# Kernel tuning notes

Measured on AMD Instinct MI355X. Metric: run time of the kernel, lower is better.

The kernel has to match this reference:

```python
import jax, jax.numpy as jnp
import numpy as np

N, E = 100000, 1600000
DIMS = [128, 64, 64, 64, 32]  # in, hid, hid, hid, out
NEG_SLOPE = 0.2               # GATv2Conv default negative_slope
ELU_ALPHA_OUT = float(DIMS[-1])  # nn.ELU(out_channels): alpha = out_channels


def setup_inputs() -> dict:
    key = jax.random.key(0)
    ks = jax.random.split(key, 16)
    inp = {
        "x": jax.random.normal(ks[0], (N, DIMS[0]), dtype=jnp.float32),
        "edge_index": jax.random.randint(ks[1], (2, E), 0, N, dtype=jnp.int64),
    }
    ki = 2
    for i in range(4):
        fin, fout = DIMS[i], DIMS[i + 1]
        s = 1.0 / np.sqrt(fin)
        inp[f"Wl{i+1}"] = jax.random.uniform(ks[ki], (fin, fout), jnp.float32, -s, s); ki += 1
        inp[f"Wr{i+1}"] = jax.random.uniform(ks[ki], (fin, fout), jnp.float32, -s, s); ki += 1
        inp[f"att{i+1}"] = jax.random.uniform(ks[ki], (fout,), jnp.float32, -s, s); ki += 1
    return inp


def gatv2_layer(x, src, dst, Wl, Wr, att):
    # single head, concat=False, no self-loops, no bias (per module config)
    xl = x @ Wl                                   # [N, F] source-side projection
    xr = x @ Wr                                   # [N, F] target-side projection
    e = jax.nn.leaky_relu(xl[src] + xr[dst], NEG_SLOPE)   # [E, F]
    score = e @ att                               # [E]
    # softmax over incoming edges of each destination node
    m = jax.ops.segment_max(score, dst, num_segments=N)    # [N]
    ex = jnp.exp(score - m[dst])                  # [E]
    denom = jax.ops.segment_sum(ex, dst, num_segments=N)   # [N]
    alpha = ex / (denom[dst] + 1e-16)             # [E]
    # scatter-add weighted source messages
    return jax.ops.segment_sum(xl[src] * alpha[:, None], dst, num_segments=N)


def reference(x, edge_index, Wl1, Wr1, att1, Wl2, Wr2, att2, Wl3, Wr3, att3, Wl4, Wr4, att4):
    src, dst = edge_index[0], edge_index[1]
    h = jax.nn.elu(gatv2_layer(x, src, dst, Wl1, Wr1, att1))
    h = jax.nn.elu(gatv2_layer(h, src, dst, Wl2, Wr2, att2))
    h = jax.nn.elu(gatv2_layer(h, src, dst, Wl3, Wr3, att3))
    h = gatv2_layer(h, src, dst, Wl4, Wr4, att4)
    # nn.ELU(out_channels) -> ELU with alpha = out_channels (faithful quirk)
    return jnp.where(h > 0, h, ELU_ALPHA_OUT * jnp.expm1(h))
```

## Files before the change

kernel.cpp:

```cpp
#include <hip/hip_runtime.h>
#include <math.h>

typedef __attribute__((ext_vector_type(8))) short bf16x8;
typedef __attribute__((ext_vector_type(4))) float f32x4;
typedef __attribute__((ext_vector_type(4))) _Float16 h4;

#define BSHIFT 7
#define CH 8192

__device__ inline unsigned short f32_to_bf16_bits(float f) {
    unsigned int u = __float_as_uint(f);
    unsigned int r = (u + 0x7fffu + ((u >> 16) & 1u)) >> 16;
    return (unsigned short)r;
}
__device__ inline float bf16_bits_to_f32(unsigned short h) {
    return __uint_as_float(((unsigned int)h) << 16);
}

#define SWZ_ADD(t, imm) \
    t += __int_as_float(__builtin_amdgcn_ds_swizzle(__float_as_int(t), imm))


__global__ __launch_bounds__(256) void bucket_hist(
    const int* __restrict__ dst, int* __restrict__ bcnt8, int E, int nb, int nbp)
{
    __shared__ int h[1024];
    for (int i = threadIdx.x; i < nb; i += 256) h[i] = 0;
    __syncthreads();
    int e0 = blockIdx.x * CH, e1 = min(e0 + CH, E);
    for (int e = e0 + (int)threadIdx.x; e < e1; e += 256)
        atomicAdd(&h[dst[e] >> BSHIFT], 1);
    __syncthreads();
    int* mycnt = bcnt8 + (blockIdx.x & 7) * nbp;
    for (int b = threadIdx.x; b < nb; b += 256) {
        int c = h[b];
        if (c) atomicAdd(&mycnt[b], c);
    }
}

__global__ void bucket_scan(const int* __restrict__ bcnt8, int* __restrict__ bbase,
                            int* __restrict__ bcur8, int* __restrict__ rowstart,
                            int nb, int nbp, int E, int N)
{
    __shared__ int sh[1024];
    int t = threadIdx.x;
    int g8[8];
    int tot = 0;
#pragma unroll
    for (int g = 0; g < 8; ++g) {
        int c = (t < nb) ? bcnt8[g * nbp + t] : 0;
        g8[g] = c; tot += c;
    }
    sh[t] = tot;
    __syncthreads();
    for (int d = 1; d < 1024; d <<= 1) {
        int a = (t >= d) ? sh[t - d] : 0;
        __syncthreads();
        sh[t] += a;
        __syncthreads();
    }
    int base = sh[t] - tot;
    if (t <= nb) bbase[t] = base;
    if (t < nb) {
        int run = base;
#pragma unroll
        for (int g = 0; g < 8; ++g) { bcur8[g * nbp + t] = run; run += g8[g]; }
    }
    if (t == 0) rowstart[N] = E;
}

__global__ __launch_bounds__(256) void bucket_scatter(
    const int* __restrict__ src, const int* __restrict__ dst,
    int* __restrict__ bcur8, unsigned* __restrict__ pairs, int E, int nb, int nbp)
{
    __shared__ int h[1024];
    for (int i = threadIdx.x; i < nb; i += 256) h[i] = 0;
    __syncthreads();
    int e0 = blockIdx.x * CH, e1 = min(e0 + CH, E);
    for (int e = e0 + (int)threadIdx.x; e < e1; e += 256)
        atomicAdd(&h[dst[e] >> BSHIFT], 1);
    __syncthreads();
    int* mycur = bcur8 + (blockIdx.x & 7) * nbp;
    for (int b = threadIdx.x; b < nb; b += 256) {
        int c = h[b];
        if (c) h[b] = atomicAdd(&mycur[b], c);
    }
    __syncthreads();
    for (int e = e0 + (int)threadIdx.x; e < e1; e += 256) {
        int d = dst[e];
        int pos = atomicAdd(&h[d >> BSHIFT], 1);
        pairs[pos] = ((unsigned)src[e] << BSHIFT) | (unsigned)(d & 127);
    }
}

__global__ __launch_bounds__(256) void bucket_finalize(
    const unsigned* __restrict__ pairs, const int* __restrict__ bbase,
    int* __restrict__ rowstart, int* __restrict__ csr_src, int N)
{
    __shared__ int h[128];
    __shared__ int sh[256];
    int b = blockIdx.x;
    int p0 = bbase[b], p1 = bbase[b + 1];
    int t = threadIdx.x;
    if (t < 128) h[t] = 0;
    __syncthreads();
    for (int e = p0 + t; e < p1; e += 256)
        atomicAdd(&h[pairs[e] & 127], 1);
    __syncthreads();
    int v = (t < 128) ? h[t] : 0;
    sh[t] = v;
    __syncthreads();
    for (int d = 1; d < 256; d <<= 1) {
        int a = (t >= d) ? sh[t - d] : 0;
        __syncthreads();
        sh[t] += a;
        __syncthreads();
    }
    if (t < 128) {
        int off = sh[t] - v;
        int node = (b << BSHIFT) + t;
        if (node < N) rowstart[node] = p0 + off;
        h[t] = p0 + off;
    }
    __syncthreads();
    for (int e = p0 + t; e < p1; e += 256) {
        unsigned pr = pairs[e];
        int pos = atomicAdd(&h[pr & 127], 1);
        csr_src[pos] = (int)(pr >> BSHIFT);
    }
}


__global__ void prepack_kernel(const float* __restrict__ Wl, const float* __restrict__ Wr,
                               unsigned short* __restrict__ pWl, unsigned short* __restrict__ pWr,
                               int FIN, int FOUT) {
    int NT = FOUT >> 4, NK = FIN >> 5;
    int part = NT * NK * 512;
    int i = blockIdx.x * blockDim.x + threadIdx.x;
    int m = i / part;
    if (m >= 2) return;
    int ii = i - m * part;
    int j = ii & 7;
    int lane = (ii >> 3) & 63;
    int rest = ii >> 9;
    int ks = rest % NK;
    int t = rest / NK;
    int k = ks * 32 + (lane >> 4) * 8 + j;
    int c = t * 16 + (lane & 15);
    const float* W = m ? Wr : Wl;
    unsigned short* P = m ? pWr : pWl;
    float w = W[(size_t)k * FOUT + c];
    unsigned short hi = f32_to_bf16_bits(w);
    unsigned short lo = f32_to_bf16_bits(w - bf16_bits_to_f32(hi));
    P[ii] = hi;
    P[part + ii] = lo;
}


template<int FIN, int FOUT>
__global__ __launch_bounds__(256) void proj_mfma_kernel(
    const float* __restrict__ x,
    const unsigned short* __restrict__ pWl, const unsigned short* __restrict__ pWr,
    const float* __restrict__ att,
    _Float16* __restrict__ xlh, float* __restrict__ xr,
    float* __restrict__ dl, float* __restrict__ dr, int n)
{
    constexpr int NT = FOUT >> 4;
    constexpr int NK = FIN >> 5;
    constexpr int PART = NT * NK * 512;
    const int wave = threadIdx.x >> 6;
    const int lane = threadIdx.x & 63;
    const int row0 = blockIdx.x * 64 + wave * 16;
    int arow = row0 + (lane & 15);
    if (arow >= n) arow = n - 1;
    const int khalf = lane >> 4;

    f32x4 accl[NT], accr[NT];
#pragma unroll
    for (int t = 0; t < NT; ++t) {
        accl[t] = (f32x4){0.f, 0.f, 0.f, 0.f};
        accr[t] = (f32x4){0.f, 0.f, 0.f, 0.f};
    }

    const float* xrow = x + (size_t)arow * FIN + khalf * 8;
#pragma unroll
    for (int ks = 0; ks < NK; ++ks) {
        float4 a0 = *(const float4*)(xrow + ks * 32);
        float4 a1 = *(const float4*)(xrow + ks * 32 + 4);
        float av[8] = {a0.x, a0.y, a0.z, a0.w, a1.x, a1.y, a1.z, a1.w};
        bf16x8 ah, al;
#pragma unroll
        for (int j = 0; j < 8; ++j) {
            unsigned short h = f32_to_bf16_bits(av[j]);
            ah[j] = (short)h;
            al[j] = (short)f32_to_bf16_bits(av[j] - bf16_bits_to_f32(h));
        }
#pragma unroll
        for (int t = 0; t < NT; ++t) {
            const unsigned short* bpl = pWl + ((size_t)(t * NK + ks) * 64 + lane) * 8;
            bf16x8 bh  = *(const bf16x8*)bpl;
            bf16x8 blo = *(const bf16x8*)(bpl + PART);
            accl[t] = __builtin_amdgcn_mfma_f32_16x16x32_bf16(ah, bh,  accl[t], 0, 0, 0);
            accl[t] = __builtin_amdgcn_mfma_f32_16x16x32_bf16(ah, blo, accl[t], 0, 0, 0);
            accl[t] = __builtin_amdgcn_mfma_f32_16x16x32_bf16(al, bh,  accl[t], 0, 0, 0);
            const unsigned short* bpr = pWr + ((size_t)(t * NK + ks) * 64 + lane) * 8;
            bh  = *(const bf16x8*)bpr;
            blo = *(const bf16x8*)(bpr + PART);
            accr[t] = __builtin_amdgcn_mfma_f32_16x16x32_bf16(ah, bh,  accr[t], 0, 0, 0);
            accr[t] = __builtin_amdgcn_mfma_f32_16x16x32_bf16(ah, blo, accr[t], 0, 0, 0);
            accr[t] = __builtin_amdgcn_mfma_f32_16x16x32_bf16(al, bh,  accr[t], 0, 0, 0);
        }
    }

    const int orow0 = row0 + khalf * 4;
    const int colb = lane & 15;
    float attc[NT];
#pragma unroll
    for (int t = 0; t < NT; ++t) attc[t] = att[t * 16 + colb];

#pragma unroll
    for (int t = 0; t < NT; ++t) {
        int col = t * 16 + colb;
#pragma unroll
        for (int r = 0; r < 4; ++r) {
            int rr = orow0 + r;
            if (rr < n) {
                xlh[(size_t)rr * FOUT + col] = (_Float16)accl[t][r];
                xr[(size_t)rr * FOUT + col] = accr[t][r];
            }
        }
    }
#pragma unroll
    for (int r = 0; r < 4; ++r) {
        float pl = 0.f, pr = 0.f;
#pragma unroll
        for (int t = 0; t < NT; ++t) { pl += accl[t][r] * attc[t]; pr += accr[t][r] * attc[t]; }
#pragma unroll
        for (int off = 1; off < 16; off <<= 1) {
            pl += __shfl_xor(pl, off);
            pr += __shfl_xor(pr, off);
        }
        int rr = orow0 + r;
        if (colb == 0 && rr < n) { dl[rr] = pl; dr[rr] = pr; }
    }
}


template<int F, int AMODE>
__global__ __launch_bounds__(256) void agg_kernel(
    const _Float16* __restrict__ xlh, const float* __restrict__ xr, const float* __restrict__ att,
    const float* __restrict__ dl, const float* __restrict__ dr,
    const int* __restrict__ rowstart, const int* __restrict__ csr_src,
    float* __restrict__ out, int n, int E)
{
    constexpr int LPE = F / 4;
    constexpr int LSH = (F == 64) ? 6 : 5;
    constexpr int NPG = 64 / LPE;

    int wv  = (blockIdx.x * blockDim.x + threadIdx.x) >> 6;
    int lane = threadIdx.x & 63;
    int grp = lane / LPE;
    int fl  = lane % LPE;
    int node = wv * NPG + grp;
    bool act = node < n;
    int nc = act ? node : 0;

    float4 xrv  = *(const float4*)&xr[((unsigned)nc << LSH) + fl * 4];
    float4 attv = *(const float4*)&att[fl * 4];
    float cdr = 0.6f * dr[nc];

    int s0 = rowstart[nc];
    int s1 = act ? rowstart[nc + 1] : s0;
    int s1c = min(max(s1 - 1, s0), E - 1);

    float m = -1e30f, mth = -1e30f, ssum = 0.f;
    float o0 = 0.f, o1 = 0.f, o2 = 0.f, o3 = 0.f;

    int ia = s0, ib = s0 + 1;
    int sva = csr_src[min(ia, s1c)];
    int svb = csr_src[min(ib, s1c)];
    float dla = dl[sva], dlb = dl[svb];
    h4 xa = *(const h4*)(xlh + (((unsigned)sva << LSH) + fl * 4));
    h4 xb = *(const h4*)(xlh + (((unsigned)svb << LSH) + fl * 4));

    while (ia < s1) {
        int nia = ia + 2, nib = ib + 2;
        int nsva = csr_src[min(nia, s1c)];
        int nsvb = csr_src[min(nib, s1c)];
        float ndla = dl[nsva], ndlb = dl[nsvb];
        h4 nxa = *(const h4*)(xlh + (((unsigned)nsva << LSH) + fl * 4));
        h4 nxb = *(const h4*)(xlh + (((unsigned)nsvb << LSH) + fl * 4));

        float xa0 = (float)xa[0], xa1 = (float)xa[1], xa2 = (float)xa[2], xa3 = (float)xa[3];
        float xb0 = (float)xb[0], xb1 = (float)xb[1], xb2 = (float)xb[2], xb3 = (float)xb[3];

        bool vb = ib < s1;
        float ta = attv.x * fabsf(xa0 + xrv.x)
                 + attv.y * fabsf(xa1 + xrv.y)
                 + attv.z * fabsf(xa2 + xrv.z)
                 + attv.w * fabsf(xa3 + xrv.w);
        float tb = attv.x * fabsf(xb0 + xrv.x)
                 + attv.y * fabsf(xb1 + xrv.y)
                 + attv.z * fabsf(xb2 + xrv.z)
                 + attv.w * fabsf(xb3 + xrv.w);
        SWZ_ADD(ta, 0x041F); SWZ_ADD(tb, 0x041F);
        SWZ_ADD(ta, 0x081F); SWZ_ADD(tb, 0x081F);
        SWZ_ADD(ta, 0x101F); SWZ_ADD(tb, 0x101F);
        if (LPE == 16) { SWZ_ADD(ta, 0x201F); SWZ_ADD(tb, 0x201F); }

        float pa = 0.6f * dla + cdr + 0.4f * ta;
        float pb = vb ? (0.6f * dlb + cdr + 0.4f * tb) : -1e30f;

        float pm = fmaxf(pa, pb);
        if (pm > mth) {
            float c = __expf(m - pm);
            ssum *= c; o0 *= c; o1 *= c; o2 *= c; o3 *= c;
            m = pm; mth = pm + 8.0f;
        }
        float wa = __expf(pa - m);
        float wb = __expf(pb - m);
        ssum += wa + wb;
        o0 += wa * xa0 + wb * xb0;
        o1 += wa * xa1 + wb * xb1;
        o2 += wa * xa2 + wb * xb2;
        o3 += wa * xa3 + wb * xb3;

        ia = nia; ib = nib;
        dla = ndla; dlb = ndlb; xa = nxa; xb = nxb;
    }

    float inv = 1.f / (ssum + 1e-16f);
    float4 res;
    res.x = o0 * inv; res.y = o1 * inv; res.z = o2 * inv; res.w = o3 * inv;
    if (AMODE == 1) {
        res.x = (res.x > 0.f) ? res.x : expm1f(res.x);
        res.y = (res.y > 0.f) ? res.y : expm1f(res.y);
        res.z = (res.z > 0.f) ? res.z : expm1f(res.z);
        res.w = (res.w > 0.f) ? res.w : expm1f(res.w);
    } else {
        res.x = (res.x > 0.f) ? res.x : 32.f * expm1f(res.x);
        res.y = (res.y > 0.f) ? res.y : 32.f * expm1f(res.y);
        res.z = (res.z > 0.f) ? res.z : 32.f * expm1f(res.z);
        res.w = (res.w > 0.f) ? res.w : 32.f * expm1f(res.w);
    }
    if (act) *(float4*)&out[((unsigned)node << LSH) + fl * 4] = res;
}


extern "C" void kernel_launch(void* const* d_in, const int* in_sizes, int n_in,
                              void* d_out, int out_size, void* d_ws, size_t ws_size,
                              hipStream_t stream) {
    const float* x    = (const float*)d_in[0];
    const int*   ei   = (const int*)d_in[1];
    const float* Wl1  = (const float*)d_in[2];
    const float* Wr1  = (const float*)d_in[3];
    const float* att1 = (const float*)d_in[4];
    const float* Wl2  = (const float*)d_in[5];
    const float* Wr2  = (const float*)d_in[6];
    const float* att2 = (const float*)d_in[7];
    const float* Wl3  = (const float*)d_in[8];
    const float* Wr3  = (const float*)d_in[9];
    const float* att3 = (const float*)d_in[10];
    const float* Wl4  = (const float*)d_in[11];
    const float* Wr4  = (const float*)d_in[12];
    const float* att4 = (const float*)d_in[13];

    const int N = in_sizes[0] / 128;
    const int E = in_sizes[1] / 2;
    const int* src = ei;
    const int* dst = ei + E;

    const int nb  = (N + 127) >> BSHIFT;
    const int nbp = (nb + 15) & ~15;

    char* w = (char*)d_ws;
    size_t off = 0;
    auto take = [&](size_t bytes) -> void* {
        void* p = w + off;
        off = (off + bytes + 255) & ~(size_t)255;
        return p;
    };
    int* bcnt8    = (int*)take((size_t)8 * nbp * 4);
    int* bcur8    = (int*)take((size_t)8 * nbp * 4);
    int* bbase    = (int*)take((size_t)(nb + 1) * 4);
    int* rowstart = (int*)take((size_t)(N + 1) * 4);
    int* csr_src  = (int*)take((size_t)E * 4);
    float* dl = (float*)take((size_t)N * 4);
    float* dr = (float*)take((size_t)N * 4);
    _Float16* xlh = (_Float16*)take((size_t)N * 64 * 2);
    float* xr = (float*)take((size_t)N * 64 * 4);
    float* hA = (float*)take((size_t)N * 64 * 4);
    float* hB = (float*)take((size_t)N * 64 * 4);
    unsigned short* pWl1 = (unsigned short*)take(2 * 4 * 4 * 512 * 2);
    unsigned short* pWr1 = (unsigned short*)take(2 * 4 * 4 * 512 * 2);
    unsigned short* pWl2 = (unsigned short*)take(2 * 4 * 2 * 512 * 2);
    unsigned short* pWr2 = (unsigned short*)take(2 * 4 * 2 * 512 * 2);
    unsigned short* pWl3 = (unsigned short*)take(2 * 4 * 2 * 512 * 2);
    unsigned short* pWr3 = (unsigned short*)take(2 * 4 * 2 * 512 * 2);
    unsigned short* pWl4 = (unsigned short*)take(2 * 2 * 2 * 512 * 2);
    unsigned short* pWr4 = (unsigned short*)take(2 * 2 * 2 * 512 * 2);
    unsigned* pairs = (unsigned*)hA;
    float* outf = (float*)d_out;

    hipMemsetAsync(bcnt8, 0, (size_t)8 * nbp * 4, stream);

    prepack_kernel<<<(2 * 4 * 4 * 512 + 255) / 256, 256, 0, stream>>>(Wl1, Wr1, pWl1, pWr1, 128, 64);
    prepack_kernel<<<(2 * 4 * 2 * 512 + 255) / 256, 256, 0, stream>>>(Wl2, Wr2, pWl2, pWr2, 64, 64);
    prepack_kernel<<<(2 * 4 * 2 * 512 + 255) / 256, 256, 0, stream>>>(Wl3, Wr3, pWl3, pWr3, 64, 64);
    prepack_kernel<<<(2 * 2 * 2 * 512 + 255) / 256, 256, 0, stream>>>(Wl4, Wr4, pWl4, pWr4, 64, 32);

    int kgrid = (E + CH - 1) / CH;
    bucket_hist<<<kgrid, 256, 0, stream>>>(dst, bcnt8, E, nb, nbp);
    bucket_scan<<<1, 1024, 0, stream>>>(bcnt8, bbase, bcur8, rowstart, nb, nbp, E, N);
    bucket_scatter<<<kgrid, 256, 0, stream>>>(src, dst, bcur8, pairs, E, nb, nbp);
    bucket_finalize<<<nb, 256, 0, stream>>>(pairs, bbase, rowstart, csr_src, N);

    int pblk = (N + 63) / 64;
    int agg64 = (N + 15) / 16;
    int agg32 = (N + 31) / 32;

    proj_mfma_kernel<128, 64><<<pblk, 256, 0, stream>>>(x, pWl1, pWr1, att1, xlh, xr, dl, dr, N);
    agg_kernel<64, 1><<<agg64, 256, 0, stream>>>(xlh, xr, att1, dl, dr, rowstart, csr_src, hA, N, E);

    proj_mfma_kernel<64, 64><<<pblk, 256, 0, stream>>>(hA, pWl2, pWr2, att2, xlh, xr, dl, dr, N);
    agg_kernel<64, 1><<<agg64, 256, 0, stream>>>(xlh, xr, att2, dl, dr, rowstart, csr_src, hB, N, E);

    proj_mfma_kernel<64, 64><<<pblk, 256, 0, stream>>>(hB, pWl3, pWr3, att3, xlh, xr, dl, dr, N);
    agg_kernel<64, 1><<<agg64, 256, 0, stream>>>(xlh, xr, att3, dl, dr, rowstart, csr_src, hA, N, E);

    proj_mfma_kernel<64, 32><<<pblk, 256, 0, stream>>>(hA, pWl4, pWr4, att4, xlh, xr, dl, dr, N);
    agg_kernel<32, 2><<<agg32, 256, 0, stream>>>(xlh, xr, att4, dl, dr, rowstart, csr_src, outf, N, E);
}
```

Baseline: 333.0 us.

## Use fp16 xr and packed half2 dot for attention scores, 8 features per lane

```diff
diff --git a/kernel.cpp b/kernel.cpp
--- a/kernel.cpp
+++ b/kernel.cpp
@@ -3,7 +3,7 @@
 
 typedef __attribute__((ext_vector_type(8))) short bf16x8;
 typedef __attribute__((ext_vector_type(4))) float f32x4;
-typedef __attribute__((ext_vector_type(4))) _Float16 h4;
+typedef __attribute__((ext_vector_type(2))) _Float16 h2;
 
 #define BSHIFT 7
 #define CH 8192
@@ -16,9 +16,23 @@
 __device__ inline float bf16_bits_to_f32(unsigned short h) {
     return __uint_as_float(((unsigned int)h) << 16);
 }
+__device__ inline h2 u2h(unsigned u) { return __builtin_bit_cast(h2, u); }
+__device__ inline unsigned h2u(h2 h) { return __builtin_bit_cast(unsigned, h); }
 
 #define SWZ_ADD(t, imm) \
     t += __int_as_float(__builtin_amdgcn_ds_swizzle(__float_as_int(t), imm))
+
+__device__ inline float dot2acc(h2 a, h2 b, float c) {
+#if defined(__has_builtin)
+#if __has_builtin(__builtin_amdgcn_fdot2)
+    return __builtin_amdgcn_fdot2(a, b, c, false);
+#else
+    return c + (float)a[0] * (float)b[0] + (float)a[1] * (float)b[1];
+#endif
+#else
+    return c + (float)a[0] * (float)b[0] + (float)a[1] * (float)b[1];
+#endif
+}
 
 
 __global__ __launch_bounds__(256) void bucket_hist(
@@ -162,7 +176,7 @@
     const float* __restrict__ x,
     const unsigned short* __restrict__ pWl, const unsigned short* __restrict__ pWr,
     const float* __restrict__ att,
-    _Float16* __restrict__ xlh, float* __restrict__ xr,
+    _Float16* __restrict__ xlh, _Float16* __restrict__ xrh,
     float* __restrict__ dl, float* __restrict__ dr, int n)
 {
     constexpr int NT = FOUT >> 4;
@@ -226,7 +240,7 @@
             int rr = orow0 + r;
             if (rr < n) {
                 xlh[(size_t)rr * FOUT + col] = (_Float16)accl[t][r];
-                xr[(size_t)rr * FOUT + col] = accr[t][r];
+                xrh[(size_t)rr * FOUT + col] = (_Float16)accr[t][r];
             }
         }
     }
@@ -248,12 +262,13 @@
 
 template<int F, int AMODE>
 __global__ __launch_bounds__(256) void agg_kernel(
-    const _Float16* __restrict__ xlh, const float* __restrict__ xr, const float* __restrict__ att,
+    const _Float16* __restrict__ xlh, const _Float16* __restrict__ xrh,
+    const float* __restrict__ att,
     const float* __restrict__ dl, const float* __restrict__ dr,
     const int* __restrict__ rowstart, const int* __restrict__ csr_src,
     float* __restrict__ out, int n, int E)
 {
-    constexpr int LPE = F / 4;
+    constexpr int LPE = F / 8;
     constexpr int LSH = (F == 64) ? 6 : 5;
     constexpr int NPG = 64 / LPE;
 
@@ -265,8 +280,16 @@
     bool act = node < n;
     int nc = act ? node : 0;
 
-    float4 xrv  = *(const float4*)&xr[((unsigned)nc << LSH) + fl * 4];
-    float4 attv = *(const float4*)&att[fl * 4];
+    float4 xrraw = *(const float4*)(xrh + (((unsigned)nc << LSH) + fl * 8));
+    h2 xrv[4];
+#pragma unroll
+    for (int j = 0; j < 4; ++j) xrv[j] = u2h(((const unsigned*)&xrraw)[j]);
+    h2 atth[4];
+#pragma unroll
+    for (int j = 0; j < 4; ++j) {
+        atth[j][0] = (_Float16)att[fl * 8 + 2 * j];
+        atth[j][1] = (_Float16)att[fl * 8 + 2 * j + 1];
+    }
     float cdr = 0.6f * dr[nc];
 
     int s0 = rowstart[nc];
@@ -274,39 +297,46 @@
     int s1c = min(max(s1 - 1, s0), E - 1);
 
     float m = -1e30f, mth = -1e30f, ssum = 0.f;
-    float o0 = 0.f, o1 = 0.f, o2 = 0.f, o3 = 0.f;
+    float o[8];
+#pragma unroll
+    for (int j = 0; j < 8; ++j) o[j] = 0.f;
 
     int ia = s0, ib = s0 + 1;
     int sva = csr_src[min(ia, s1c)];
     int svb = csr_src[min(ib, s1c)];
     float dla = dl[sva], dlb = dl[svb];
-    h4 xa = *(const h4*)(xlh + (((unsigned)sva << LSH) + fl * 4));
-    h4 xb = *(const h4*)(xlh + (((unsigned)svb << LSH) + fl * 4));
+    float4 rawa = *(const float4*)(xlh + (((unsigned)sva << LSH) + fl * 8));
+    float4 rawb = *(const float4*)(xlh + (((unsigned)svb << LSH) + fl * 8));
 
     while (ia < s1) {
         int nia = ia + 2, nib = ib + 2;
         int nsva = csr_src[min(nia, s1c)];
         int nsvb = csr_src[min(nib, s1c)];
         float ndla = dl[nsva], ndlb = dl[nsvb];
-        h4 nxa = *(const h4*)(xlh + (((unsigned)nsva << LSH) + fl * 4));
-        h4 nxb = *(const h4*)(xlh + (((unsigned)nsvb << LSH) + fl * 4));
-
-        float xa0 = (float)xa[0], xa1 = (float)xa[1], xa2 = (float)xa[2], xa3 = (float)xa[3];
-        float xb0 = (float)xb[0], xb1 = (float)xb[1], xb2 = (float)xb[2], xb3 = (float)xb[3];
+        float4 nrawa = *(const float4*)(xlh + (((unsigned)nsva << LSH) + fl * 8));
+        float4 nrawb = *(const float4*)(xlh + (((unsigned)nsvb << LSH) + fl * 8));
+
+        h2 a[4], b[4];
+#pragma unroll
+        for (int j = 0; j < 4; ++j) {
+            a[j] = u2h(((const unsigned*)&rawa)[j]);
+            b[j] = u2h(((const unsigned*)&rawb)[j]);
+        }
 
         bool vb = ib < s1;
-        float ta = attv.x * fabsf(xa0 + xrv.x)
-                 + attv.y * fabsf(xa1 + xrv.y)
-                 + attv.z * fabsf(xa2 + xrv.z)
-                 + attv.w * fabsf(xa3 + xrv.w);
-        float tb = attv.x * fabsf(xb0 + xrv.x)
-                 + attv.y * fabsf(xb1 + xrv.y)
-                 + attv.z * fabsf(xb2 + xrv.z)
-                 + attv.w * fabsf(xb3 + xrv.w);
+        float ta = 0.f, tb = 0.f;
+#pragma unroll
+        for (int j = 0; j < 4; ++j) {
+            h2 ea = a[j] + xrv[j];
+            h2 eb = b[j] + xrv[j];
+            ea = u2h(h2u(ea) & 0x7FFF7FFFu);
+            eb = u2h(h2u(eb) & 0x7FFF7FFFu);
+            ta = dot2acc(atth[j], ea, ta);
+            tb = dot2acc(atth[j], eb, tb);
+        }
         SWZ_ADD(ta, 0x041F); SWZ_ADD(tb, 0x041F);
         SWZ_ADD(ta, 0x081F); SWZ_ADD(tb, 0x081F);
-        SWZ_ADD(ta, 0x101F); SWZ_ADD(tb, 0x101F);
-        if (LPE == 16) { SWZ_ADD(ta, 0x201F); SWZ_ADD(tb, 0x201F); }
+        if (LPE == 8) { SWZ_ADD(ta, 0x101F); SWZ_ADD(tb, 0x101F); }
 
         float pa = 0.6f * dla + cdr + 0.4f * ta;
         float pb = vb ? (0.6f * dlb + cdr + 0.4f * tb) : -1e30f;
@@ -314,36 +344,38 @@
         float pm = fmaxf(pa, pb);
         if (pm > mth) {
             float c = __expf(m - pm);
-            ssum *= c; o0 *= c; o1 *= c; o2 *= c; o3 *= c;
+            ssum *= c;
+#pragma unroll
+            for (int j = 0; j < 8; ++j) o[j] *= c;
             m = pm; mth = pm + 8.0f;
         }
         float wa = __expf(pa - m);
         float wb = __expf(pb - m);
         ssum += wa + wb;
-        o0 += wa * xa0 + wb * xb0;
-        o1 += wa * xa1 + wb * xb1;
-        o2 += wa * xa2 + wb * xb2;
-        o3 += wa * xa3 + wb * xb3;
+#pragma unroll
+        for (int j = 0; j < 4; ++j) {
+            o[2 * j]     += wa * (float)a[j][0] + wb * (float)b[j][0];
+            o[2 * j + 1] += wa * (float)a[j][1] + wb * (float)b[j][1];
+        }
 
         ia = nia; ib = nib;
-        dla = ndla; dlb = ndlb; xa = nxa; xb = nxb;
+        dla = ndla; dlb = ndlb; rawa = nrawa; rawb = nrawb;
     }
 
     float inv = 1.f / (ssum + 1e-16f);
-    float4 res;
-    res.x = o0 * inv; res.y = o1 * inv; res.z = o2 * inv; res.w = o3 * inv;
-    if (AMODE == 1) {
-        res.x = (res.x > 0.f) ? res.x : expm1f(res.x);
-        res.y = (res.y > 0.f) ? res.y : expm1f(res.y);
-        res.z = (res.z > 0.f) ? res.z : expm1f(res.z);
-        res.w = (res.w > 0.f) ? res.w : expm1f(res.w);
-    } else {
-        res.x = (res.x > 0.f) ? res.x : 32.f * expm1f(res.x);
-        res.y = (res.y > 0.f) ? res.y : 32.f * expm1f(res.y);
-        res.z = (res.z > 0.f) ? res.z : 32.f * expm1f(res.z);
-        res.w = (res.w > 0.f) ? res.w : 32.f * expm1f(res.w);
-    }
-    if (act) *(float4*)&out[((unsigned)node << LSH) + fl * 4] = res;
+    float res[8];
+#pragma unroll
+    for (int j = 0; j < 8; ++j) {
+        float r = o[j] * inv;
+        if (AMODE == 1) r = (r > 0.f) ? r : expm1f(r);
+        else            r = (r > 0.f) ? r : 32.f * expm1f(r);
+        res[j] = r;
+    }
+    if (act) {
+        float* op = out + (((unsigned)node << LSH) + fl * 8);
+        *(float4*)op       = (float4){res[0], res[1], res[2], res[3]};
+        *(float4*)(op + 4) = (float4){res[4], res[5], res[6], res[7]};
+    }
 }
 
 
@@ -388,7 +420,7 @@
     float* dl = (float*)take((size_t)N * 4);
     float* dr = (float*)take((size_t)N * 4);
     _Float16* xlh = (_Float16*)take((size_t)N * 64 * 2);
-    float* xr = (float*)take((size_t)N * 64 * 4);
+    _Float16* xrh = (_Float16*)take((size_t)N * 64 * 2);
     float* hA = (float*)take((size_t)N * 64 * 4);
     float* hB = (float*)take((size_t)N * 64 * 4);
     unsigned short* pWl1 = (unsigned short*)take(2 * 4 * 4 * 512 * 2);
@@ -416,18 +448,18 @@
     bucket_finalize<<<nb, 256, 0, stream>>>(pairs, bbase, rowstart, csr_src, N);
 
     int pblk = (N + 63) / 64;
-    int agg64 = (N + 15) / 16;
-    int agg32 = (N + 31) / 32;
-
-    proj_mfma_kernel<128, 64><<<pblk, 256, 0, stream>>>(x, pWl1, pWr1, att1, xlh, xr, dl, dr, N);
-    agg_kernel<64, 1><<<agg64, 256, 0, stream>>>(xlh, xr, att1, dl, dr, rowstart, csr_src, hA, N, E);
-
-    proj_mfma_kernel<64, 64><<<pblk, 256, 0, stream>>>(hA, pWl2, pWr2, att2, xlh, xr, dl, dr, N);
-    agg_kernel<64, 1><<<agg64, 256, 0, stream>>>(xlh, xr, att2, dl, dr, rowstart, csr_src, hB, N, E);
-
-    proj_mfma_kernel<64, 64><<<pblk, 256, 0, stream>>>(hB, pWl3, pWr3, att3, xlh, xr, dl, dr, N);
-    agg_kernel<64, 1><<<agg64, 256, 0, stream>>>(xlh, xr, att3, dl, dr, rowstart, csr_src, hA, N, E);
-
-    proj_mfma_kernel<64, 32><<<pblk, 256, 0, stream>>>(hA, pWl4, pWr4, att4, xlh, xr, dl, dr, N);
-    agg_kernel<32, 2><<<agg32, 256, 0, stream>>>(xlh, xr, att4, dl, dr, rowstart, csr_src, outf, N, E);
-}
+    int agg64 = (N + 31) / 32;
+    int agg32 = (N + 63) / 64;
+
+    proj_mfma_kernel<128, 64><<<pblk, 256, 0, stream>>>(x, pWl1, pWr1, att1, xlh, xrh, dl, dr, N);
+    agg_kernel<64, 1><<<agg64, 256, 0, stream>>>(xlh, xrh, att1, dl, dr, rowstart, csr_src, hA, N, E);
+
+    proj_mfma_kernel<64, 64><<<pblk, 256, 0, stream>>>(hA, pWl2, pWr2, att2, xlh, xrh, dl, dr, N);
+    agg_kernel<64, 1><<<agg64, 256, 0, stream>>>(xlh, xrh, att2, dl, dr, rowstart, csr_src, hB, N, E);
+
+    proj_mfma_kernel<64, 64><<<pblk, 256, 0, stream>>>(hB, pWl3, pWr3, att3, xlh, xrh, dl, dr, N);
+    agg_kernel<64, 1><<<agg64, 256, 0, stream>>>(xlh, xrh, att3, dl, dr, rowstart, csr_src, hA, N, E);
+
+    proj_mfma_kernel<64, 32><<<pblk, 256, 0, stream>>>(hA, pWl4, pWr4, att4, xlh, xrh, dl, dr, N);
+    agg_kernel<32, 2><<<agg32, 256, 0, stream>>>(xlh, xrh, att4, dl, dr, rowstart, csr_src, outf, N, E);
+}
```

After: 304.6 us. 8.6% less time.
